# Kernel tuning notes

Hardware: AMD Instinct MI355X
Metric: run time of the kernel (lower is better)

## Reference

```python
import jax, jax.numpy as jnp
import numpy as np

M = 2048  # pooled grid rows (init arg m)
N = 2048  # pooled grid cols (init arg n); code requires m == n


def setup_inputs() -> dict:
    key = jax.random.key(0)
    d_coarse = jax.random.normal(key, (2 * M, 2 * N), dtype=jnp.float32)
    return {"d_coarse": d_coarse}


def reference(d_coarse):
    m, n = M, N
    # MaxPool2d(kernel_size=2, stride=2) on the (2m, 2n) coarse depth map -> (m, n)
    d_pool = d_coarse.reshape(m, 2, n, 2).max(axis=(1, 3))

    k_noise, k_drop = jax.random.split(jax.random.key(1))
    # Noise module: torch.rand_like * stdev(1) + mean(0)  (uniform [0,1) noise)
    noise = jax.random.uniform(k_noise, d_pool.shape, dtype=d_pool.dtype)
    d_noised = d_pool + noise

    # IntervalThreshold: (max - min) / min(m, n)
    thr = (jnp.max(d_pool) - jnp.min(d_pool)) / min(m, n)

    rows = jnp.arange(m)[:, None]  # i index
    cols = jnp.arange(n)[None, :]  # j index
    adj = jnp.zeros((m, n), dtype=bool)

    # ReconGraph: only diagonal offsets survive (dx != 0 and dy != 0),
    # i.e. (dx, dy) in {-1, 1}^2. For each (i, j) compare d[i+dy, j+dx] vs d[i, j].
    for dx in (-1, 1):
        for dy in (-1, 1):
            # shifted[i, j] == d_noised[i + dy, j + dx]
            shifted = jnp.roll(d_noised, shift=(-dy, -dx), axis=(0, 1))
            ok = jnp.abs(shifted - d_noised) <= thr
            # Original boundary conditions, plus in-range guards on the
            # actually-accessed indices (i+dy, j+dx).
            mask = ((rows + dx >= 0) & (rows + dy < m)
                    & (cols + dx >= 0) & (cols + dy < n)
                    & (rows + dy >= 0) & (cols + dx < n))
            # Write goes to adjacency_matrix[j, i] -> transpose (m == n).
            adj = adj | (ok & mask).T

    # GraphDropout with p=0.5: bernoulli keep mask on the boolean matrix
    # (self.train is the bound method -> truthy, so dropout always applies).
    keep = jax.random.bernoulli(k_drop, 0.5, adj.shape)
    return adj & keep
```

## Files before the change

kernel.cpp:

```cpp
#include <hip/hip_runtime.h>

typedef unsigned int u32;

#define HALF_T 2097152u
#define NPX 2048

__host__ __device__ inline void tf2x32(u32 k0, u32 k1, u32& x0, u32& x1) {
  const u32 ks2 = k0 ^ k1 ^ 0x1BD11BDAu;
  x0 += k0; x1 += k1;
#define TFR(r) { x0 += x1; x1 = (x1 << (r)) | (x1 >> (32 - (r))); x1 ^= x0; }
  TFR(13) TFR(15) TFR(26) TFR(6)
  x0 += k1;  x1 += ks2 + 1u;
  TFR(17) TFR(29) TFR(16) TFR(24)
  x0 += ks2; x1 += k0 + 2u;
  TFR(13) TFR(15) TFR(26) TFR(6)
  x0 += k0;  x1 += k1 + 3u;
  TFR(17) TFR(29) TFR(16) TFR(24)
  x0 += k1;  x1 += ks2 + 4u;
  TFR(13) TFR(15) TFR(26) TFR(6)
  x0 += ks2; x1 += k0 + 5u;
#undef TFR
}

__device__ inline u32 pbits(u32 k0, u32 k1, u32 t) {
  u32 x0 = 0u, x1 = t;
  tf2x32(k0, k1, x0, x1);
  return x0 ^ x1;
}

__device__ inline float bits_to_uniform(u32 bits) {
  return __uint_as_float((bits >> 9) | 0x3F800000u) - 1.0f;
}

template<bool STORE>
__global__ __launch_bounds__(256) void k_pool(const float* __restrict__ coarse,
                                              float* __restrict__ dn,
                                              float* __restrict__ pmin,
                                              float* __restrict__ pmax,
                                              u32 kn0, u32 kn1) {
  float lmin = INFINITY, lmax = -INFINITY;
  const int stride = gridDim.x * 256;
  for (u32 t = blockIdx.x * 256 + threadIdx.x; t < HALF_T; t += stride) {
    const int i = t >> 11, j = t & 2047;
    const float2* r0 = (const float2*)(coarse + (size_t)(2*i    ) * 4096);
    const float2* r1 = (const float2*)(coarse + (size_t)(2*i + 1) * 4096);
    float2 a = r0[j], b = r1[j];
    float p0 = fmaxf(fmaxf(a.x, a.y), fmaxf(b.x, b.y));
    const float2* r2 = (const float2*)(coarse + (size_t)(2*i + 2048) * 4096);
    const float2* r3 = (const float2*)(coarse + (size_t)(2*i + 2049) * 4096);
    float2 c = r2[j], d = r3[j];
    float p1 = fmaxf(fmaxf(c.x, c.y), fmaxf(d.x, d.y));
    lmin = fminf(lmin, fminf(p0, p1));
    lmax = fmaxf(lmax, fmaxf(p0, p1));
    if (STORE) {
      dn[t]          = p0 + bits_to_uniform(pbits(kn0, kn1, t));
      dn[t + HALF_T] = p1 + bits_to_uniform(pbits(kn0, kn1, t + HALF_T));
    }
  }
  for (int off = 32; off > 0; off >>= 1) {
    lmin = fminf(lmin, __shfl_down(lmin, off, 64));
    lmax = fmaxf(lmax, __shfl_down(lmax, off, 64));
  }
  __shared__ float smin[4], smax[4];
  const int lane = threadIdx.x & 63, wv = threadIdx.x >> 6;
  if (lane == 0) { smin[wv] = lmin; smax[wv] = lmax; }
  __syncthreads();
  if (threadIdx.x == 0) {
    pmin[blockIdx.x] = fminf(fminf(smin[0], smin[1]), fminf(smin[2], smin[3]));
    pmax[blockIdx.x] = fmaxf(fmaxf(smax[0], smax[1]), fmaxf(smax[2], smax[3]));
  }
}

__global__ __launch_bounds__(256) void k_final(const float* __restrict__ pmin,
                                               const float* __restrict__ pmax,
                                               float* __restrict__ thr, int nblk) {
  float lmin = INFINITY, lmax = -INFINITY;
  for (int i = threadIdx.x; i < nblk; i += 256) {
    lmin = fminf(lmin, pmin[i]);
    lmax = fmaxf(lmax, pmax[i]);
  }
  for (int off = 32; off > 0; off >>= 1) {
    lmin = fminf(lmin, __shfl_down(lmin, off, 64));
    lmax = fmaxf(lmax, __shfl_down(lmax, off, 64));
  }
  __shared__ float smin[4], smax[4];
  const int lane = threadIdx.x & 63, wv = threadIdx.x >> 6;
  if (lane == 0) { smin[wv] = lmin; smax[wv] = lmax; }
  __syncthreads();
  if (threadIdx.x == 0) {
    float gmin = fminf(fminf(smin[0], smin[1]), fminf(smin[2], smin[3]));
    float gmax = fmaxf(fmaxf(smax[0], smax[1]), fmaxf(smax[2], smax[3]));
    thr[0] = (gmax - gmin) / 2048.0f;
  }
}

__device__ inline bool adj_eval(const float s[34][35], int tx, int ty,
                                int c, int rr, float thr) {
  const float ctr = s[tx+1][ty+1];
  const bool cge1 = (c  >= 1),    cle = (c  <= NPX - 2);
  const bool rge1 = (rr >= 1),    rle = (rr <= NPX - 2);
  bool a = false;
  if (cge1 && rge1)                    a |= (fabsf(s[tx  ][ty  ] - ctr) <= thr);
  if (cge1 && cle && rge1 && rle)      a |= (fabsf(s[tx+2][ty  ] - ctr) <= thr);
  if (cge1 && rle)                     a |= (fabsf(s[tx  ][ty+2] - ctr) <= thr);
  if (cle  && rle)                     a |= (fabsf(s[tx+2][ty+2] - ctr) <= thr);
  return a;
}

__global__ __launch_bounds__(1024) void k_graph(const float* __restrict__ dn,
                                                const float* __restrict__ thrp,
                                                int* __restrict__ out,
                                                u32 kd0, u32 kd1) {
  __shared__ float s0[34][35];
  __shared__ float s1[34][35];
  const float thr = *thrp;
  const int c0 = blockIdx.x * 32, r0 = blockIdx.y * 32;
  const int tid = threadIdx.y * 32 + threadIdx.x;
  for (int idx = tid; idx < 34 * 34; idx += 1024) {
    const int lc = idx / 34, lr = idx - lc * 34;
    const int c = c0 - 1 + lc;
    const int r = r0 - 1 + lr;
    float v0 = 0.f, v1 = 0.f;
    if ((unsigned)c < (unsigned)NPX) {
      if ((unsigned)r < (unsigned)NPX)          v0 = dn[c * NPX + r];
      const int r2 = r + 1024;
      if ((unsigned)r2 < (unsigned)NPX)         v1 = dn[c * NPX + r2];
    }
    s0[lc][lr] = v0;
    s1[lc][lr] = v1;
  }
  __syncthreads();
  const int tx = threadIdx.x, ty = threadIdx.y;
  const int c = c0 + tx, r = r0 + ty;
  const bool adj0 = adj_eval(s0, tx, ty, c, r,        thr);
  const bool adj1 = adj_eval(s1, tx, ty, c, r + 1024, thr);
  const u32 t0 = (u32)(r * NPX + c);
  const bool keep0 = !(pbits(kd0, kd1, t0)          >> 31);
  const bool keep1 = !(pbits(kd0, kd1, t0 + HALF_T) >> 31);
  out[(size_t)r * NPX + c]          = (adj0 && keep0) ? 1 : 0;
  out[(size_t)(r + 1024) * NPX + c] = (adj1 && keep1) ? 1 : 0;
}

__device__ inline float dn_compute(const float* __restrict__ coarse,
                                   int i, int j, u32 kn0, u32 kn1) {
  const float2* r0 = (const float2*)(coarse + (size_t)(2*i    ) * 4096);
  const float2* r1 = (const float2*)(coarse + (size_t)(2*i + 1) * 4096);
  float2 a = r0[j], b = r1[j];
  float p = fmaxf(fmaxf(a.x, a.y), fmaxf(b.x, b.y));
  return p + bits_to_uniform(pbits(kn0, kn1, (u32)(i * NPX + j)));
}

__global__ __launch_bounds__(1024) void k_graph_fused(const float* __restrict__ coarse,
                                                      const float* __restrict__ thrp,
                                                      int* __restrict__ out,
                                                      u32 kn0, u32 kn1, u32 kd0, u32 kd1) {
  __shared__ float s0[34][35];
  __shared__ float s1[34][35];
  const float thr = *thrp;
  const int c0 = blockIdx.x * 32, r0 = blockIdx.y * 32;
  const int tid = threadIdx.y * 32 + threadIdx.x;
  for (int idx = tid; idx < 34 * 34; idx += 1024) {
    const int lc = idx / 34, lr = idx - lc * 34;
    const int c = c0 - 1 + lc;
    const int r = r0 - 1 + lr;
    float v0 = 0.f, v1 = 0.f;
    if ((unsigned)c < (unsigned)NPX) {
      if ((unsigned)r < (unsigned)NPX)      v0 = dn_compute(coarse, c, r, kn0, kn1);
      const int r2 = r + 1024;
      if ((unsigned)r2 < (unsigned)NPX)     v1 = dn_compute(coarse, c, r2, kn0, kn1);
    }
    s0[lc][lr] = v0;
    s1[lc][lr] = v1;
  }
  __syncthreads();
  const int tx = threadIdx.x, ty = threadIdx.y;
  const int c = c0 + tx, r = r0 + ty;
  const bool adj0 = adj_eval(s0, tx, ty, c, r,        thr);
  const bool adj1 = adj_eval(s1, tx, ty, c, r + 1024, thr);
  const u32 t0 = (u32)(r * NPX + c);
  const bool keep0 = !(pbits(kd0, kd1, t0)          >> 31);
  const bool keep1 = !(pbits(kd0, kd1, t0 + HALF_T) >> 31);
  out[(size_t)r * NPX + c]          = (adj0 && keep0) ? 1 : 0;
  out[(size_t)(r + 1024) * NPX + c] = (adj1 && keep1) ? 1 : 0;
}

extern "C" void kernel_launch(void* const* d_in, const int* in_sizes, int n_in,
                              void* d_out, int out_size, void* d_ws, size_t ws_size,
                              hipStream_t stream) {
  const float* coarse = (const float*)d_in[0];
  int* out = (int*)d_out;

  u32 a0 = 0u, a1 = 0u; tf2x32(0u, 1u, a0, a1);
  u32 b0 = 0u, b1 = 1u; tf2x32(0u, 1u, b0, b1);
  const u32 kn0 = a0, kn1 = a1, kd0 = b0, kd1 = b1;

  char* ws = (char*)d_ws;
  float* thr  = (float*)ws;
  float* pmin = (float*)(ws + 64);
  float* pmax = (float*)(ws + 64 + 8192);
  const size_t dn_off = 32768;
  const size_t dn_bytes = (size_t)NPX * NPX * sizeof(float);
  const bool stored = ws_size >= dn_off + dn_bytes;

  if (stored) {
    float* dn = (float*)(ws + dn_off);
    k_pool<true><<<2048, 256, 0, stream>>>(coarse, dn, pmin, pmax, kn0, kn1);
    k_final<<<1, 256, 0, stream>>>(pmin, pmax, thr, 2048);
    k_graph<<<dim3(64, 32), dim3(32, 32), 0, stream>>>(dn, thr, out, kd0, kd1);
  } else {
    k_pool<false><<<2048, 256, 0, stream>>>(coarse, nullptr, pmin, pmax, kn0, kn1);
    k_final<<<1, 256, 0, stream>>>(pmin, pmax, thr, 2048);
    k_graph_fused<<<dim3(64, 32), dim3(32, 32), 0, stream>>>(coarse, thr, out,
                                                             kn0, kn1, kd0, kd1);
  }
}
```

Baseline: 118.2 us.

## Drop final reduction kernel, fold threshold into graph blocks, vectorize pool loads

Removes the single-block k_final launch. Each graph block now reduces the 4096 per-block partial min/max values itself to derive the threshold. The pool kernel switches to one thread per two output pixels using float4 loads and float2 stores, with no grid-stride loop. This saves a launch and a serial tiny kernel, at the cost of every graph block redundantly reading 32 KB of partials.

```diff
diff --git a/kernel.cpp b/kernel.cpp
--- a/kernel.cpp
+++ b/kernel.cpp
@@ -4,6 +4,7 @@
 
 #define HALF_T 2097152u
 #define NPX 2048
+#define NPOOL_BLOCKS 4096
 
 __host__ __device__ inline void tf2x32(u32 k0, u32 k1, u32& x0, u32& x1) {
   const u32 ks2 = k0 ^ k1 ^ 0x1BD11BDAu;
@@ -32,31 +33,38 @@
   return __uint_as_float((bits >> 9) | 0x3F800000u) - 1.0f;
 }
 
-template<bool STORE>
 __global__ __launch_bounds__(256) void k_pool(const float* __restrict__ coarse,
-                                              float* __restrict__ dn,
+                                              float2* __restrict__ dn2,
                                               float* __restrict__ pmin,
                                               float* __restrict__ pmax,
                                               u32 kn0, u32 kn1) {
-  float lmin = INFINITY, lmax = -INFINITY;
-  const int stride = gridDim.x * 256;
-  for (u32 t = blockIdx.x * 256 + threadIdx.x; t < HALF_T; t += stride) {
-    const int i = t >> 11, j = t & 2047;
-    const float2* r0 = (const float2*)(coarse + (size_t)(2*i    ) * 4096);
-    const float2* r1 = (const float2*)(coarse + (size_t)(2*i + 1) * 4096);
-    float2 a = r0[j], b = r1[j];
-    float p0 = fmaxf(fmaxf(a.x, a.y), fmaxf(b.x, b.y));
-    const float2* r2 = (const float2*)(coarse + (size_t)(2*i + 2048) * 4096);
-    const float2* r3 = (const float2*)(coarse + (size_t)(2*i + 2049) * 4096);
-    float2 c = r2[j], d = r3[j];
-    float p1 = fmaxf(fmaxf(c.x, c.y), fmaxf(d.x, d.y));
-    lmin = fminf(lmin, fminf(p0, p1));
-    lmax = fmaxf(lmax, fmaxf(p0, p1));
-    if (STORE) {
-      dn[t]          = p0 + bits_to_uniform(pbits(kn0, kn1, t));
-      dn[t + HALF_T] = p1 + bits_to_uniform(pbits(kn0, kn1, t + HALF_T));
-    }
-  }
+  const u32 g = blockIdx.x * 256 + threadIdx.x;
+  const int i  = g >> 10;
+  const int jj = g & 1023;
+
+  const float4* r0 = (const float4*)(coarse + (size_t)(2*i       ) * 4096);
+  const float4* r1 = (const float4*)(coarse + (size_t)(2*i + 1   ) * 4096);
+  const float4* r2 = (const float4*)(coarse + (size_t)(2*i + 2048) * 4096);
+  const float4* r3 = (const float4*)(coarse + (size_t)(2*i + 2049) * 4096);
+  const float4 a = r0[jj], b = r1[jj], c = r2[jj], d = r3[jj];
+
+  const float p0a = fmaxf(fmaxf(a.x, a.y), fmaxf(b.x, b.y));
+  const float p0b = fmaxf(fmaxf(a.z, a.w), fmaxf(b.z, b.w));
+  const float p1a = fmaxf(fmaxf(c.x, c.y), fmaxf(d.x, d.y));
+  const float p1b = fmaxf(fmaxf(c.z, c.w), fmaxf(d.z, d.w));
+
+  float lmin = fminf(fminf(p0a, p0b), fminf(p1a, p1b));
+  float lmax = fmaxf(fmaxf(p0a, p0b), fmaxf(p1a, p1b));
+
+  const u32 t0 = (u32)i * 2048u + 2u * (u32)jj;
+  const u32 t2 = t0 + HALF_T;
+  dn2[(size_t)i * 1024 + jj] =
+      make_float2(p0a + bits_to_uniform(pbits(kn0, kn1, t0)),
+                  p0b + bits_to_uniform(pbits(kn0, kn1, t0 + 1u)));
+  dn2[(size_t)(i + 1024) * 1024 + jj] =
+      make_float2(p1a + bits_to_uniform(pbits(kn0, kn1, t2)),
+                  p1b + bits_to_uniform(pbits(kn0, kn1, t2 + 1u)));
+
   for (int off = 32; off > 0; off >>= 1) {
     lmin = fminf(lmin, __shfl_down(lmin, off, 64));
     lmax = fmaxf(lmax, __shfl_down(lmax, off, 64));
@@ -71,27 +79,34 @@
   }
 }
 
-__global__ __launch_bounds__(256) void k_final(const float* __restrict__ pmin,
-                                               const float* __restrict__ pmax,
-                                               float* __restrict__ thr, int nblk) {
+__device__ inline float block_thr(const float* __restrict__ pmin,
+                                  const float* __restrict__ pmax,
+                                  int tid) {
+  __shared__ float smin[16], smax[16], sthr;
   float lmin = INFINITY, lmax = -INFINITY;
-  for (int i = threadIdx.x; i < nblk; i += 256) {
-    lmin = fminf(lmin, pmin[i]);
-    lmax = fmaxf(lmax, pmax[i]);
+#pragma unroll
+  for (int k = 0; k < NPOOL_BLOCKS; k += 1024) {
+    lmin = fminf(lmin, pmin[tid + k]);
+    lmax = fmaxf(lmax, pmax[tid + k]);
   }
   for (int off = 32; off > 0; off >>= 1) {
     lmin = fminf(lmin, __shfl_down(lmin, off, 64));
     lmax = fmaxf(lmax, __shfl_down(lmax, off, 64));
   }
-  __shared__ float smin[4], smax[4];
-  const int lane = threadIdx.x & 63, wv = threadIdx.x >> 6;
+  const int lane = tid & 63, wv = tid >> 6;
   if (lane == 0) { smin[wv] = lmin; smax[wv] = lmax; }
   __syncthreads();
-  if (threadIdx.x == 0) {
-    float gmin = fminf(fminf(smin[0], smin[1]), fminf(smin[2], smin[3]));
-    float gmax = fmaxf(fmaxf(smax[0], smax[1]), fmaxf(smax[2], smax[3]));
-    thr[0] = (gmax - gmin) / 2048.0f;
-  }
+  if (tid == 0) {
+    float gmin = smin[0], gmax = smax[0];
+#pragma unroll
+    for (int w = 1; w < 16; ++w) {
+      gmin = fminf(gmin, smin[w]);
+      gmax = fmaxf(gmax, smax[w]);
+    }
+    sthr = (gmax - gmin) / 2048.0f;
+  }
+  __syncthreads();
+  return sthr;
 }
 
 __device__ inline bool adj_eval(const float s[34][35], int tx, int ty,
@@ -108,14 +123,16 @@
 }
 
 __global__ __launch_bounds__(1024) void k_graph(const float* __restrict__ dn,
-                                                const float* __restrict__ thrp,
+                                                const float* __restrict__ pmin,
+                                                const float* __restrict__ pmax,
                                                 int* __restrict__ out,
                                                 u32 kd0, u32 kd1) {
   __shared__ float s0[34][35];
   __shared__ float s1[34][35];
-  const float thr = *thrp;
+  const int tid = threadIdx.y * 32 + threadIdx.x;
+  const float thr = block_thr(pmin, pmax, tid);
+
   const int c0 = blockIdx.x * 32, r0 = blockIdx.y * 32;
-  const int tid = threadIdx.y * 32 + threadIdx.x;
   for (int idx = tid; idx < 34 * 34; idx += 1024) {
     const int lc = idx / 34, lr = idx - lc * 34;
     const int c = c0 - 1 + lc;
@@ -141,6 +158,39 @@
   out[(size_t)(r + 1024) * NPX + c] = (adj1 && keep1) ? 1 : 0;
 }
 
+__global__ __launch_bounds__(256) void k_pool_nostore(const float* __restrict__ coarse,
+                                                      float* __restrict__ pmin,
+                                                      float* __restrict__ pmax) {
+  const u32 g = blockIdx.x * 256 + threadIdx.x;
+  const int i  = g >> 10;
+  const int jj = g & 1023;
+  const float4* r0 = (const float4*)(coarse + (size_t)(2*i       ) * 4096);
+  const float4* r1 = (const float4*)(coarse + (size_t)(2*i + 1   ) * 4096);
+  const float4* r2 = (const float4*)(coarse + (size_t)(2*i + 2048) * 4096);
+  const float4* r3 = (const float4*)(coarse + (size_t)(2*i + 2049) * 4096);
+  const float4 a = r0[jj], b = r1[jj], c = r2[jj], d = r3[jj];
+  float lmin = fminf(fminf(fmaxf(fmaxf(a.x,a.y),fmaxf(b.x,b.y)),
+                           fmaxf(fmaxf(a.z,a.w),fmaxf(b.z,b.w))),
+                     fminf(fmaxf(fmaxf(c.x,c.y),fmaxf(d.x,d.y)),
+                           fmaxf(fmaxf(c.z,c.w),fmaxf(d.z,d.w))));
+  float lmax = fmaxf(fmaxf(fmaxf(fmaxf(a.x,a.y),fmaxf(b.x,b.y)),
+                           fmaxf(fmaxf(a.z,a.w),fmaxf(b.z,b.w))),
+                     fmaxf(fmaxf(fmaxf(c.x,c.y),fmaxf(d.x,d.y)),
+                           fmaxf(fmaxf(c.z,c.w),fmaxf(d.z,d.w))));
+  for (int off = 32; off > 0; off >>= 1) {
+    lmin = fminf(lmin, __shfl_down(lmin, off, 64));
+    lmax = fmaxf(lmax, __shfl_down(lmax, off, 64));
+  }
+  __shared__ float smin[4], smax[4];
+  const int lane = threadIdx.x & 63, wv = threadIdx.x >> 6;
+  if (lane == 0) { smin[wv] = lmin; smax[wv] = lmax; }
+  __syncthreads();
+  if (threadIdx.x == 0) {
+    pmin[blockIdx.x] = fminf(fminf(smin[0], smin[1]), fminf(smin[2], smin[3]));
+    pmax[blockIdx.x] = fmaxf(fmaxf(smax[0], smax[1]), fmaxf(smax[2], smax[3]));
+  }
+}
+
 __device__ inline float dn_compute(const float* __restrict__ coarse,
                                    int i, int j, u32 kn0, u32 kn1) {
   const float2* r0 = (const float2*)(coarse + (size_t)(2*i    ) * 4096);
@@ -151,14 +201,15 @@
 }
 
 __global__ __launch_bounds__(1024) void k_graph_fused(const float* __restrict__ coarse,
-                                                      const float* __restrict__ thrp,
+                                                      const float* __restrict__ pmin,
+                                                      const float* __restrict__ pmax,
                                                       int* __restrict__ out,
                                                       u32 kn0, u32 kn1, u32 kd0, u32 kd1) {
   __shared__ float s0[34][35];
   __shared__ float s1[34][35];
-  const float thr = *thrp;
+  const int tid = threadIdx.y * 32 + threadIdx.x;
+  const float thr = block_thr(pmin, pmax, tid);
   const int c0 = blockIdx.x * 32, r0 = blockIdx.y * 32;
-  const int tid = threadIdx.y * 32 + threadIdx.x;
   for (int idx = tid; idx < 34 * 34; idx += 1024) {
     const int lc = idx / 34, lr = idx - lc * 34;
     const int c = c0 - 1 + lc;
@@ -195,22 +246,19 @@
   const u32 kn0 = a0, kn1 = a1, kd0 = b0, kd1 = b1;
 
   char* ws = (char*)d_ws;
-  float* thr  = (float*)ws;
-  float* pmin = (float*)(ws + 64);
-  float* pmax = (float*)(ws + 64 + 8192);
+  float* pmin = (float*)ws;
+  float* pmax = (float*)(ws + 16384);
   const size_t dn_off = 32768;
   const size_t dn_bytes = (size_t)NPX * NPX * sizeof(float);
   const bool stored = ws_size >= dn_off + dn_bytes;
 
   if (stored) {
     float* dn = (float*)(ws + dn_off);
-    k_pool<true><<<2048, 256, 0, stream>>>(coarse, dn, pmin, pmax, kn0, kn1);
-    k_final<<<1, 256, 0, stream>>>(pmin, pmax, thr, 2048);
-    k_graph<<<dim3(64, 32), dim3(32, 32), 0, stream>>>(dn, thr, out, kd0, kd1);
+    k_pool<<<NPOOL_BLOCKS, 256, 0, stream>>>(coarse, (float2*)dn, pmin, pmax, kn0, kn1);
+    k_graph<<<dim3(64, 32), dim3(32, 32), 0, stream>>>(dn, pmin, pmax, out, kd0, kd1);
   } else {
-    k_pool<false><<<2048, 256, 0, stream>>>(coarse, nullptr, pmin, pmax, kn0, kn1);
-    k_final<<<1, 256, 0, stream>>>(pmin, pmax, thr, 2048);
-    k_graph_fused<<<dim3(64, 32), dim3(32, 32), 0, stream>>>(coarse, thr, out,
+    k_pool_nostore<<<NPOOL_BLOCKS, 256, 0, stream>>>(coarse, pmin, pmax);
+    k_graph_fused<<<dim3(64, 32), dim3(32, 32), 0, stream>>>(coarse, pmin, pmax, out,
                                                              kn0, kn1, kd0, kd1);
   }
 }
```

Result: no change. 117.7 us (-0.4%).
